# Kernel tuning notes

Hardware: AMD Instinct MI355X
Metric: run time of the kernel (lower is better)

Reference implementation:

```python
import jax, jax.numpy as jnp
import numpy as np

B, C, NQ, NK, S, H, FF = 8, 256, 1024, 4096, 16, 8, 2048
DH = C // H
EPS = 1e-5


def _layernorm(x, g, b):
    m = jnp.mean(x, axis=-1, keepdims=True)
    v = jnp.mean((x - m) ** 2, axis=-1, keepdims=True)
    return (x - m) * jax.lax.rsqrt(v + EPS) * g + b


def _box_query(key_pos, query_pos):
    # key_pos: (B,NK,3); query_pos: (B,NQ,6) = centers ++ box sizes (L,H,W)
    centers = query_pos[:, :, None, :3]            # (B,NQ,1,3)
    half = 0.5 * query_pos[:, :, None, 3:]         # (B,NQ,1,3)
    off = jnp.abs(key_pos[:, None, :, :] - centers)  # (B,NQ,NK,3)
    inside = jnp.all(off <= half, axis=-1)         # (B,NQ,NK)
    # first n_sample inside-points in index order (stable sort: inside first)
    order = jnp.argsort(~inside, axis=-1, stable=True)
    idx = order[..., :S]                           # (B,NQ,S)
    valid = jnp.take_along_axis(inside, idx, axis=-1)
    mask = ~valid                                  # True = padded / masked
    idx = jnp.where(mask, 0, idx)
    mask = mask.at[..., 0].set(False)              # matches cuda path: slot 0 never masked
    return idx, mask


def _forward(query, key, query_pos, key_pos,
             q_w, q_b, k_w, k_b, v_w, v_b, o_w, o_b,
             lin1_w, lin1_b, lin2_w, lin2_b,
             n1_g, n1_b, n2_g, n2_b, qpe_w, qpe_b, kpe_w, kpe_b):
    idx, mask = _box_query(key_pos, query_pos)     # (B,NQ,S), (B,NQ,S)
    # gather neighborhoods
    gxyz = jax.vmap(lambda kp, ix: kp[ix])(key_pos, idx)        # (B,NQ,S,3)
    gxyz = gxyz - query_pos[:, :, None, :3]                     # center-relative
    gfeat = jax.vmap(lambda kf, ix: kf[:, ix])(key, idx)        # (B,C,NQ,S)

    BQ = B * NQ
    kfeat = jnp.transpose(gfeat, (0, 2, 3, 1)).reshape(BQ, S, C)   # (BQ,S,C)
    kpe = gxyz.reshape(BQ, S, 3) @ kpe_w.T + kpe_b                 # cross_embed
    qtok = jnp.transpose(query, (0, 2, 1)).reshape(BQ, C)          # (BQ,C)
    qpe = (query_pos @ qpe_w.T + qpe_b).reshape(BQ, C)             # pos_embed

    # multihead cross-attention: 1 query vs S=16 local keys per group
    kv_in = kfeat + kpe
    qh = ((qtok + qpe) @ q_w.T + q_b).reshape(BQ, H, DH)
    kh = (kv_in @ k_w.T + k_b).reshape(BQ, S, H, DH)
    vh = (kv_in @ v_w.T + v_b).reshape(BQ, S, H, DH)
    scores = jnp.einsum('bhd,bshd->bhs', qh, kh) / np.sqrt(DH)    # (BQ,H,S)
    scores = jnp.where(mask.reshape(BQ, 1, S), -1e30, scores)
    attn = jax.nn.softmax(scores, axis=-1)
    ao = jnp.einsum('bhs,bshd->bhd', attn, vh).reshape(BQ, C)
    ao = ao @ o_w.T + o_b

    x = _layernorm(qtok + ao, n1_g, n1_b)                         # post-norm
    ff = jax.nn.relu(x @ lin1_w.T + lin1_b) @ lin2_w.T + lin2_b
    x = _layernorm(x + ff, n2_g, n2_b)
    return jnp.transpose(x.reshape(B, NQ, C), (0, 2, 1))          # (B,C,NQ)


def setup_inputs() -> dict:
    rng = jax.random.key(0)
    ks = jax.random.split(rng, 24)
    s = 0.02
    query = jax.random.normal(ks[0], (B, C, NQ), jnp.float32)
    key = jax.random.normal(ks[1], (B, C, NK), jnp.float32)
    key_pos = jax.random.uniform(ks[2], (B, NK, 3), jnp.float32)
    centers = jax.random.uniform(ks[3], (B, NQ, 3), jnp.float32)
    sizes = jax.random.uniform(ks[4], (B, NQ, 3), jnp.float32, minval=0.1, maxval=0.4)
    query_pos = jnp.concatenate([centers, sizes], axis=-1)
    p = {
        'q_w': jax.random.normal(ks[5], (C, C)) * s, 'q_b': jnp.zeros((C,)),
        'k_w': jax.random.normal(ks[6], (C, C)) * s, 'k_b': jnp.zeros((C,)),
        'v_w': jax.random.normal(ks[7], (C, C)) * s, 'v_b': jnp.zeros((C,)),
        'o_w': jax.random.normal(ks[8], (C, C)) * s, 'o_b': jnp.zeros((C,)),
        'lin1_w': jax.random.normal(ks[9], (FF, C)) * s, 'lin1_b': jnp.zeros((FF,)),
        'lin2_w': jax.random.normal(ks[10], (C, FF)) * s, 'lin2_b': jnp.zeros((C,)),
        'n1_g': jnp.ones((C,)), 'n1_b': jnp.zeros((C,)),
        'n2_g': jnp.ones((C,)), 'n2_b': jnp.zeros((C,)),
        'qpe_w': jax.random.normal(ks[11], (C, 6)) * s, 'qpe_b': jnp.zeros((C,)),
        'kpe_w': jax.random.normal(ks[12], (C, 3)) * s, 'kpe_b': jnp.zeros((C,)),
    }
    return dict(query=query, key=key, query_pos=query_pos, key_pos=key_pos, **p)


def reference(query, key, query_pos, key_pos,
              q_w, q_b, k_w, k_b, v_w, v_b, o_w, o_b,
              lin1_w, lin1_b, lin2_w, lin2_b,
              n1_g, n1_b, n2_g, n2_b, qpe_w, qpe_b, kpe_w, kpe_b):
    return _forward(query, key, query_pos, key_pos,
                    q_w, q_b, k_w, k_b, v_w, v_b, o_w, o_b,
                    lin1_w, lin1_b, lin2_w, lin2_b,
                    n1_g, n1_b, n2_g, n2_b, qpe_w, qpe_b, kpe_w, kpe_b)
```

## Files before the change

### kernel.cpp

```cpp
#include <hip/hip_runtime.h>
#include <cstdint>

#define B_   8
#define C_   256
#define NQ_  1024
#define NK_  4096
#define S_   16
#define H_   8
#define FF_  2048
#define DH_  32
#define BQ_  (B_*NQ_)
#define EPS_ 1e-5f
#define KS_  8

typedef __bf16 bf16x8 __attribute__((ext_vector_type(8)));
typedef __bf16 bf16x4 __attribute__((ext_vector_type(4)));
typedef float  f32x4  __attribute__((ext_vector_type(4)));

struct CvtArgs {
  const float* src[6];
  __bf16* dst[6];
};

#define SEGA 2048
#define SEGB 10240
#define SEGC 12288
#define SEGD 13568
#define NPREP 13584

__global__ __launch_bounds__(256) void k_prep(
    const float* __restrict__ query, const float* __restrict__ key,
    const float* __restrict__ query_pos, const float* __restrict__ key_pos,
    const float* __restrict__ qpe_w, const float* __restrict__ qpe_b,
    const float* __restrict__ k_w, const float* __restrict__ k_b,
    const float* __restrict__ v_w, const float* __restrict__ v_b,
    const float* __restrict__ kpe_w, const float* __restrict__ kpe_b,
    CvtArgs ca,
    __bf16* __restrict__ keyTb, __bf16* __restrict__ qtokb,
    __bf16* __restrict__ qinb,
    float4* __restrict__ Pk, float4* __restrict__ Pv,
    int* __restrict__ idxo, int* __restrict__ masko) {
  __shared__ __align__(16) float smem[1248];
  int blk = blockIdx.x, t = threadIdx.x;
  int tx = t & 31, ty = t >> 5;

  if (blk < SEGA) {
    int lane = t & 63;
    int q = blk * 4 + (t >> 6);
    int b = q >> 10;
    const float* kpb = key_pos + (size_t)b * NK_ * 3;
    const float* qp = query_pos + (size_t)q * 6;
    float cx = qp[0], cy = qp[1], cz = qp[2];
    float hx = 0.5f * qp[3], hy = 0.5f * qp[4], hz = 0.5f * qp[5];
    int* iq = idxo + (size_t)q * S_;
    int found = 0;
    for (int ch = 0; ch < NK_ / 64; ch += 4) {
      float dx[4], dy[4], dz[4];
#pragma unroll
      for (int u = 0; u < 4; ++u) {
        int k = (ch + u) * 64 + lane;
        dx[u] = fabsf(kpb[k * 3 + 0] - cx);
        dy[u] = fabsf(kpb[k * 3 + 1] - cy);
        dz[u] = fabsf(kpb[k * 3 + 2] - cz);
      }
#pragma unroll
      for (int u = 0; u < 4; ++u) {
        bool inside = (dx[u] <= hx) && (dy[u] <= hy) && (dz[u] <= hz);
        unsigned long long bal = __ballot(inside);
        if (inside) {
          int slot = found + __popcll(bal & ((1ull << lane) - 1ull));
          if (slot < S_) iq[slot] = (ch + u) * 64 + lane;
        }
        found += __popcll(bal);
      }
      if (found >= S_) break;
    }
    if (found > S_) found = S_;
    if (lane < S_) {
      int m = (lane < found) ? 0 : 1;
      if (lane >= found) iq[lane] = 0;
      if (lane == 0) m = 0;
      masko[(size_t)q * S_ + lane] = m;
    }
  } else if (blk < SEGB) {
    int local = blk - SEGA;
    float (*tt)[33] = (float(*)[33])smem;
    int x = local & 127, y = (local >> 7) & 7, z = local >> 10;
    int j0 = x * 32, i0 = y * 32;
    const float* inz = key + (size_t)z * C_ * NK_;
    __bf16* outz = keyTb + (size_t)z * NK_ * C_;
#pragma unroll
    for (int r = 0; r < 32; r += 8)
      tt[ty + r][tx] = inz[(size_t)(i0 + ty + r) * NK_ + (j0 + tx)];
    __syncthreads();
#pragma unroll
    for (int r = 0; r < 32; r += 8)
      outz[(size_t)(j0 + ty + r) * C_ + (i0 + tx)] = (__bf16)tt[tx][ty + r];
  } else if (blk < SEGC) {
    int local = blk - SEGB;
    float (*tt)[33] = (float(*)[33])smem;
    float (*sqp)[6] = (float(*)[6])(smem + 1056);
    int x = local & 31, y = (local >> 5) & 7, z = local >> 8;
    int nq0 = x * 32, c0 = y * 32;
    const float* inz = query + (size_t)z * C_ * NQ_;
#pragma unroll
    for (int r = 0; r < 32; r += 8)
      tt[ty + r][tx] = inz[(size_t)(c0 + ty + r) * NQ_ + (nq0 + tx)];
    if (t < 192)
      sqp[t / 6][t % 6] = query_pos[((size_t)z * NQ_ + nq0 + t / 6) * 6 + (t % 6)];
    int c = c0 + tx;
    float w0 = qpe_w[c * 6 + 0], w1 = qpe_w[c * 6 + 1], w2 = qpe_w[c * 6 + 2];
    float w3 = qpe_w[c * 6 + 3], w4 = qpe_w[c * 6 + 4], w5 = qpe_w[c * 6 + 5];
    float wb = qpe_b[c];
    __syncthreads();
#pragma unroll
    for (int r = 0; r < 32; r += 8) {
      int nql = ty + r;
      size_t row = (size_t)z * NQ_ + nq0 + nql;
      float v = tt[tx][nql];
      float pe = wb + sqp[nql][0] * w0 + sqp[nql][1] * w1 + sqp[nql][2] * w2 +
                 sqp[nql][3] * w3 + sqp[nql][4] * w4 + sqp[nql][5] * w5;
      qtokb[row * C_ + c] = (__bf16)v;
      qinb[row * C_ + c] = (__bf16)(v + pe);
    }
  } else if (blk < SEGD) {
    int local = blk - SEGC;
    int idx, base;
    if (local < 64)       { idx = 0; base = local; }
    else if (local < 128) { idx = 1; base = local - 64; }
    else if (local < 192) { idx = 2; base = local - 128; }
    else if (local < 256) { idx = 3; base = local - 192; }
    else if (local < 768) { idx = 4; base = local - 256; }
    else                  { idx = 5; base = local - 768; }
    size_t off = (size_t)base * 1024 + t * 4;
    float4 v = *(const float4*)(ca.src[idx] + off);
    __bf16* o = ca.dst[idx] + off;
    o[0] = (__bf16)v.x; o[1] = (__bf16)v.y; o[2] = (__bf16)v.z; o[3] = (__bf16)v.w;
  } else {
    int local = blk - SEGD;
    int bx = local & 7, bv = local >> 3;
    const float* w  = bv ? v_w : k_w;
    const float* wb = bv ? v_b : k_b;
    float4* P = bv ? Pv : Pk;
    float4 (*red)[8] = (float4(*)[8])smem;
    int nl = t >> 3, ks = (t & 7) * 32;
    int n = bx * 32 + nl;
    const float* wr = w + (size_t)n * C_;
    float p0 = 0.f, p1 = 0.f, p2 = 0.f, pb = 0.f;
#pragma unroll
    for (int k = ks; k < ks + 32; ++k) {
      float wv = wr[k];
      p0 += kpe_w[k * 3 + 0] * wv;
      p1 += kpe_w[k * 3 + 1] * wv;
      p2 += kpe_w[k * 3 + 2] * wv;
      pb += kpe_b[k] * wv;
    }
    red[nl][t & 7] = make_float4(p0, p1, p2, pb);
    __syncthreads();
    if (t < 32) {
      float4 s = red[t][0];
#pragma unroll
      for (int j = 1; j < 8; ++j) {
        float4 r = red[t][j];
        s.x += r.x; s.y += r.y; s.z += r.z; s.w += r.w;
      }
      s.w += wb[bx * 32 + t];
      P[bx * 32 + t] = s;
    }
  }
}

template <int BM, int BN, int RELU, int OUT_BF16>
__device__ __forceinline__ void gemm_body(
    const __bf16* __restrict__ A, const __bf16* __restrict__ Wn,
    const float* __restrict__ bias, void* __restrict__ outp,
    int n0, int m0, int N, int K, int kbeg, int kend) {
  constexpr int MI = BM / 32, JN = BN / 32;
  constexpr int AIT = (BM * 64) / 2048, BIT = (BN * 64) / 2048;
  __shared__ __bf16 As[BM][72];
  __shared__ __bf16 Bs[BN][72];
  int t = threadIdx.x;
  int lane = t & 63, w = t >> 6;
  int lane16 = lane & 15, quad = lane >> 4;
  int wm = (w & 1) * (BM / 2), wn = (w >> 1) * (BN / 2);

  f32x4 acc[MI][JN];
#pragma unroll
  for (int i = 0; i < MI; ++i)
#pragma unroll
    for (int j = 0; j < JN; ++j) acc[i][j] = (f32x4){0.f, 0.f, 0.f, 0.f};

  for (int k0 = kbeg; k0 < kend; k0 += 64) {
#pragma unroll
    for (int i = 0; i < AIT; ++i) {
      int ii = i * 256 + t;
      int m = ii >> 3, kc = (ii & 7) * 8;
      *(bf16x8*)&As[m][kc] = *(const bf16x8*)&A[(size_t)(m0 + m) * K + k0 + kc];
    }
#pragma unroll
    for (int i = 0; i < BIT; ++i) {
      int ii = i * 256 + t;
      int m = ii >> 3, kc = (ii & 7) * 8;
      *(bf16x8*)&Bs[m][kc] = *(const bf16x8*)&Wn[(size_t)(n0 + m) * K + k0 + kc];
    }
    __syncthreads();
#pragma unroll
    for (int kk = 0; kk < 64; kk += 32) {
      bf16x8 af[MI], bfr[JN];
#pragma unroll
      for (int i = 0; i < MI; ++i)
        af[i] = *(const bf16x8*)&As[wm + i * 16 + lane16][kk + quad * 8];
#pragma unroll
      for (int j = 0; j < JN; ++j)
        bfr[j] = *(const bf16x8*)&Bs[wn + j * 16 + lane16][kk + quad * 8];
#pragma unroll
      for (int i = 0; i < MI; ++i)
#pragma unroll
        for (int j = 0; j < JN; ++j)
          acc[i][j] = __builtin_amdgcn_mfma_f32_16x16x32_bf16(af[i], bfr[j], acc[i][j], 0, 0, 0);
    }
    __syncthreads();
  }

#pragma unroll
  for (int j = 0; j < JN; ++j) {
    int col = n0 + wn + j * 16 + lane16;
    float bv = bias ? bias[col] : 0.f;
#pragma unroll
    for (int i = 0; i < MI; ++i) {
#pragma unroll
      for (int r = 0; r < 4; ++r) {
        int row = m0 + wm + i * 16 + quad * 4 + r;
        float v = acc[i][j][r] + bv;
        if (RELU) v = fmaxf(v, 0.f);
        if (OUT_BF16)
          ((__bf16*)outp)[(size_t)row * N + col] = (__bf16)v;
        else
          ((float*)outp)[(size_t)row * N + col] = v;
      }
    }
  }
}

template <int BM, int BN, int RELU, int OUT_BF16>
__global__ __launch_bounds__(256) void k_gemm(
    const __bf16* __restrict__ A, const __bf16* __restrict__ Wn,
    const float* __restrict__ bias, void* __restrict__ outp, int N, int K) {
  gemm_body<BM, BN, RELU, OUT_BF16>(A, Wn, bias, outp,
                                    blockIdx.x * BN, blockIdx.y * BM, N, K, 0, K);
}

__global__ __launch_bounds__(256) void k_gemmsk(
    const __bf16* __restrict__ A, const __bf16* __restrict__ Wn,
    __bf16* __restrict__ partials) {
  int ks = blockIdx.z;
  int kbeg = ks * (FF_ / KS_), kend = kbeg + FF_ / KS_;
  gemm_body<128, 128, 0, 1>(A, Wn, nullptr,
                            partials + (size_t)ks * BQ_ * C_,
                            blockIdx.x * 128, blockIdx.y * 128, C_, FF_, kbeg, kend);
}

__global__ __launch_bounds__(256) void k_gemmsko(
    const __bf16* __restrict__ A, const __bf16* __restrict__ Wn,
    __bf16* __restrict__ partials) {
  int ks = blockIdx.z;
  int kbeg = ks * 128, kend = kbeg + 128;
  gemm_body<128, 64, 0, 1>(A, Wn, nullptr,
                           partials + (size_t)ks * BQ_ * C_,
                           blockIdx.x * 64, blockIdx.y * 128, C_, C_, kbeg, kend);
}

__global__ __launch_bounds__(256) void k_gemm2(
    const __bf16* __restrict__ keyTb, const __bf16* __restrict__ kvwb,
    __bf16* __restrict__ khvbuf,
    const __bf16* __restrict__ qinb, const __bf16* __restrict__ qwb,
    const float* __restrict__ q_b, __bf16* __restrict__ qhb) {
  int blk = blockIdx.x;
  const __bf16 *A, *Wn; const float* bias; __bf16* outp; int n0, m0, N;
  if (blk < 1024) {
    A = keyTb; Wn = kvwb; bias = nullptr; outp = khvbuf;
    n0 = (blk & 3) * 128; m0 = (blk >> 2) * 128; N = 512;
  } else {
    int l = blk - 1024;
    A = qinb; Wn = qwb; bias = q_b; outp = qhb;
    n0 = (l & 1) * 128; m0 = (l >> 1) * 128; N = 256;
  }
  gemm_body<128, 128, 0, 1>(A, Wn, bias, outp, n0, m0, N, 256, 0, 256);
}

__global__ __launch_bounds__(256) void k_attnf(
    const __bf16* __restrict__ khv,
    const float* __restrict__ key_pos,
    const float* __restrict__ query_pos,
    const int* __restrict__ idx,
    const int* __restrict__ maskb,
    const __bf16* __restrict__ qhb,
    const float4* __restrict__ Pk,
    const float4* __restrict__ Pv,
    __bf16* __restrict__ aob) {
  __shared__ __bf16 kvs[S_][520];
  __shared__ float qrow[C_];
  __shared__ float sc[H_][S_];
  __shared__ float pw[H_][S_];
  __shared__ float4 gx4[S_];
  __shared__ float4 pgxs[H_];
  __shared__ float4 qpks[H_];
  __shared__ int srow[S_], smask[S_];
  int bq = blockIdx.x, b = bq >> 10, t = threadIdx.x;

  if (t < S_) {
    int k = idx[(size_t)bq * S_ + t];
    srow[t] = b * NK_ + k;
    smask[t] = maskb[(size_t)bq * S_ + t];
    const float* kpp = key_pos + ((size_t)b * NK_ + k) * 3;
    const float* qp  = query_pos + (size_t)bq * 6;
    gx4[t] = make_float4(kpp[0] - qp[0], kpp[1] - qp[1], kpp[2] - qp[2], 1.f);
  }
  float qv_t = (float)qhb[(size_t)bq * C_ + t];
  qrow[t] = qv_t;
  {
    float4 p = Pk[t];
    p.x *= qv_t; p.y *= qv_t; p.z *= qv_t; p.w *= qv_t;
#pragma unroll
    for (int off = 16; off >= 1; off >>= 1) {
      p.x += __shfl_xor(p.x, off);
      p.y += __shfl_xor(p.y, off);
      p.z += __shfl_xor(p.z, off);
      p.w += __shfl_xor(p.w, off);
    }
    if ((t & 31) == 0) {
      const float s = 0.17677669529663687f;
      qpks[t >> 5] = make_float4(p.x * s, p.y * s, p.z * s, p.w * s);
    }
  }
  __syncthreads();
  {
    int s = t >> 4, c0 = (t & 15) * 32;
    const __bf16* src = khv + (size_t)srow[s] * 512 + c0;
    *(bf16x8*)&kvs[s][c0]      = *(const bf16x8*)&src[0];
    *(bf16x8*)&kvs[s][c0 + 8]  = *(const bf16x8*)&src[8];
    *(bf16x8*)&kvs[s][c0 + 16] = *(const bf16x8*)&src[16];
    *(bf16x8*)&kvs[s][c0 + 24] = *(const bf16x8*)&src[24];
  }
  __syncthreads();
  if (t < H_ * S_) {
    int h = t >> 4, s = t & (S_ - 1);
    float d = 0.f;
#pragma unroll
    for (int c0 = 0; c0 < 32; c0 += 8) {
      bf16x8 xv = *(const bf16x8*)&kvs[s][h * 32 + c0];
#pragma unroll
      for (int j = 0; j < 8; ++j) d += qrow[h * 32 + c0 + j] * (float)xv[j];
    }
    d *= 0.17677669529663687f;
    float4 g = gx4[s];
    float4 pk = qpks[h];
    d += g.x * pk.x + g.y * pk.y + g.z * pk.z + pk.w;
    if (smask[s]) d = -1e30f;
    sc[h][s] = d;
  }
  __syncthreads();
  if (t < H_) {
    float mx = -3.4e38f;
#pragma unroll
    for (int s = 0; s < S_; ++s) mx = fmaxf(mx, sc[t][s]);
    float e[S_], sum = 0.f;
#pragma unroll
    for (int s = 0; s < S_; ++s) { e[s] = expf(sc[t][s] - mx); sum += e[s]; }
    float inv = 1.f / sum;
    float gxx = 0.f, gyy = 0.f, gzz = 0.f;
#pragma unroll
    for (int s = 0; s < S_; ++s) {
      float p = e[s] * inv;
      pw[t][s] = p;
      float4 g = gx4[s];
      gxx += p * g.x; gyy += p * g.y; gzz += p * g.z;
    }
    pgxs[t] = make_float4(gxx, gyy, gzz, 1.f);
  }
  __syncthreads();
  {
    int h = t >> 5;
    float a = 0.f;
#pragma unroll
    for (int s = 0; s < S_; ++s) a += pw[h][s] * (float)kvs[s][256 + t];
    float4 pv = Pv[t];
    float4 g = pgxs[h];
    a += g.x * pv.x + g.y * pv.y + g.z * pv.z + pv.w;
    aob[(size_t)bq * C_ + t] = (__bf16)a;
  }
}

__global__ __launch_bounds__(256) void k_ln1(const __bf16* __restrict__ xa,
                                             const __bf16* __restrict__ op2,
                                             const float* __restrict__ obias,
                                             const float* __restrict__ g,
                                             const float* __restrict__ bb,
                                             __bf16* __restrict__ outb) {
  int wid = (blockIdx.x * 256 + threadIdx.x) >> 6;
  int lane = threadIdx.x & 63;
  bf16x4 va = *(const bf16x4*)&xa[(size_t)wid * C_ + lane * 4];
  float4 ob4 = *(const float4*)(obias + lane * 4);
  bf16x4 p0 = *(const bf16x4*)&op2[(size_t)wid * C_ + lane * 4];
  bf16x4 p1 = *(const bf16x4*)&op2[(size_t)BQ_ * C_ + (size_t)wid * C_ + lane * 4];
  float x0 = (float)va[0] + ob4.x + (float)p0[0] + (float)p1[0];
  float x1 = (float)va[1] + ob4.y + (float)p0[1] + (float)p1[1];
  float x2 = (float)va[2] + ob4.z + (float)p0[2] + (float)p1[2];
  float x3 = (float)va[3] + ob4.w + (float)p0[3] + (float)p1[3];
  float s = x0 + x1 + x2 + x3;
#pragma unroll
  for (int off = 32; off >= 1; off >>= 1) s += __shfl_xor(s, off);
  float mean = s * (1.f / C_);
  float d0 = x0 - mean, d1 = x1 - mean, d2 = x2 - mean, d3 = x3 - mean;
  float v = d0 * d0 + d1 * d1 + d2 * d2 + d3 * d3;
#pragma unroll
  for (int off = 32; off >= 1; off >>= 1) v += __shfl_xor(v, off);
  float inv = 1.f / sqrtf(v * (1.f / C_) + EPS_);
  float4 g4 = *(const float4*)(g + lane * 4);
  float4 b4 = *(const float4*)(bb + lane * 4);
  __bf16* obp = outb + (size_t)wid * C_ + lane * 4;
  obp[0] = (__bf16)(d0 * inv * g4.x + b4.x);
  obp[1] = (__bf16)(d1 * inv * g4.y + b4.y);
  obp[2] = (__bf16)(d2 * inv * g4.z + b4.z);
  obp[3] = (__bf16)(d3 * inv * g4.w + b4.w);
}

__global__ __launch_bounds__(256) void k_lnt(const __bf16* __restrict__ x1b,
                                             const __bf16* __restrict__ ff2p,
                                             const float* __restrict__ l2bias,
                                             const float* __restrict__ g,
                                             const float* __restrict__ bb,
                                             float* __restrict__ out) {
  __shared__ float buf[32][257];
  int z = blockIdx.y, nq0 = blockIdx.x * 32;
  int t = threadIdx.x;
  int w = t >> 6, lane = t & 63;
  float4 g4 = *(const float4*)(g + lane * 4);
  float4 b4 = *(const float4*)(bb + lane * 4);
  float4 l2b = *(const float4*)(l2bias + lane * 4);
#pragma unroll
  for (int rr = 0; rr < 8; ++rr) {
    int row = w * 8 + rr;
    size_t grow = (size_t)z * NQ_ + nq0 + row;
    bf16x4 va = *(const bf16x4*)&x1b[grow * C_ + lane * 4];
    float x0 = (float)va[0] + l2b.x, x1 = (float)va[1] + l2b.y;
    float x2 = (float)va[2] + l2b.z, x3 = (float)va[3] + l2b.w;
#pragma unroll
    for (int ks = 0; ks < KS_; ++ks) {
      bf16x4 p = *(const bf16x4*)&ff2p[((size_t)ks * BQ_ + grow) * C_ + lane * 4];
      x0 += (float)p[0]; x1 += (float)p[1]; x2 += (float)p[2]; x3 += (float)p[3];
    }
    float s = x0 + x1 + x2 + x3;
#pragma unroll
    for (int off = 32; off >= 1; off >>= 1) s += __shfl_xor(s, off);
    float mean = s * (1.f / C_);
    float d0 = x0 - mean, d1 = x1 - mean, d2 = x2 - mean, d3 = x3 - mean;
    float v = d0 * d0 + d1 * d1 + d2 * d2 + d3 * d3;
#pragma unroll
    for (int off = 32; off >= 1; off >>= 1) v += __shfl_xor(v, off);
    float inv = 1.f / sqrtf(v * (1.f / C_) + EPS_);
    buf[row][lane * 4 + 0] = d0 * inv * g4.x + b4.x;
    buf[row][lane * 4 + 1] = d1 * inv * g4.y + b4.y;
    buf[row][lane * 4 + 2] = d2 * inv * g4.z + b4.z;
    buf[row][lane * 4 + 3] = d3 * inv * g4.w + b4.w;
  }
  __syncthreads();
  int tx = t & 31, ty = t >> 5;
#pragma unroll
  for (int ci = 0; ci < 32; ++ci) {
    int c = ci * 8 + ty;
    out[((size_t)z * C_ + c) * NQ_ + nq0 + tx] = buf[tx][c];
  }
}

extern "C" void kernel_launch(void* const* d_in, const int* in_sizes, int n_in,
                              void* d_out, int out_size, void* d_ws, size_t ws_size,
                              hipStream_t stream) {
  const float* query     = (const float*)d_in[0];
  const float* key       = (const float*)d_in[1];
  const float* query_pos = (const float*)d_in[2];
  const float* key_pos   = (const float*)d_in[3];
  const float* q_w = (const float*)d_in[4];  const float* q_b = (const float*)d_in[5];
  const float* k_w = (const float*)d_in[6];  const float* k_b = (const float*)d_in[7];
  const float* v_w = (const float*)d_in[8];  const float* v_b = (const float*)d_in[9];
  const float* o_w = (const float*)d_in[10]; const float* o_b = (const float*)d_in[11];
  const float* lin1_w = (const float*)d_in[12]; const float* lin1_b = (const float*)d_in[13];
  const float* lin2_w = (const float*)d_in[14]; const float* lin2_b = (const float*)d_in[15];
  const float* n1_g = (const float*)d_in[16]; const float* n1_b = (const float*)d_in[17];
  const float* n2_g = (const float*)d_in[18]; const float* n2_b = (const float*)d_in[19];
  const float* qpe_w = (const float*)d_in[20]; const float* qpe_b = (const float*)d_in[21];
  const float* kpe_w = (const float*)d_in[22]; const float* kpe_b = (const float*)d_in[23];
  float* out = (float*)d_out;

  const size_t BQc = (size_t)BQ_ * C_;
  float* w = (float*)d_ws;
  size_t o = 0;
  __bf16* keyTb = (__bf16*)(w + o); o += (size_t)B_ * NK_ * C_ / 2;
  __bf16* qtokb = (__bf16*)(w + o); o += BQc / 2;
  __bf16* op2  = (__bf16*)(w + o); o += BQc;
  __bf16* khvbuf = (__bf16*)(w + o); o += (size_t)B_ * NK_ * 512 / 2;
  __bf16* ff2p = (__bf16*)(w + o); o += BQc * KS_ / 2;
  __bf16* qinb = (__bf16*)(w + o); o += BQc / 2;
  __bf16* qhb  = (__bf16*)(w + o); o += BQc / 2;
  __bf16* aob  = (__bf16*)(w + o); o += BQc / 2;
  __bf16* x1b  = (__bf16*)(w + o); o += BQc / 2;
  __bf16* qwb  = (__bf16*)(w + o); o += (size_t)C_ * C_ / 2;
  __bf16* kvwb = (__bf16*)(w + o); o += (size_t)C_ * C_;
  __bf16* owb  = (__bf16*)(w + o); o += (size_t)C_ * C_ / 2;
  __bf16* l1b  = (__bf16*)(w + o); o += (size_t)C_ * FF_ / 2;
  __bf16* l2b  = (__bf16*)(w + o); o += (size_t)C_ * FF_ / 2;
  float4* Pk   = (float4*)(w + o); o += C_ * 4;
  float4* Pv   = (float4*)(w + o); o += C_ * 4;
  int* idxb  = (int*)(w + o); o += (size_t)BQ_ * S_;
  int* maskb = (int*)(w + o); o += (size_t)BQ_ * S_;
  __bf16* ff1b = khvbuf;

  CvtArgs ca;
  ca.src[0] = q_w; ca.dst[0] = qwb;
  ca.src[1] = k_w; ca.dst[1] = kvwb;
  ca.src[2] = v_w; ca.dst[2] = kvwb + (size_t)C_ * C_;
  ca.src[3] = o_w; ca.dst[3] = owb;
  ca.src[4] = lin1_w; ca.dst[4] = l1b;
  ca.src[5] = lin2_w; ca.dst[5] = l2b;
  k_prep<<<NPREP, 256, 0, stream>>>(query, key, query_pos, key_pos,
                                    qpe_w, qpe_b, k_w, k_b, v_w, v_b,
                                    kpe_w, kpe_b, ca,
                                    keyTb, qtokb, qinb, Pk, Pv, idxb, maskb);
  k_gemm2<<<1024 + 128, 256, 0, stream>>>(keyTb, kvwb, khvbuf, qinb, qwb, q_b, qhb);
  k_attnf<<<BQ_, 256, 0, stream>>>(khvbuf, key_pos, query_pos, idxb, maskb,
                                   qhb, Pk, Pv, aob);
  k_gemmsko<<<dim3(C_ / 64, BQ_ / 128, 2), 256, 0, stream>>>(aob, owb, op2);
  k_ln1<<<BQ_ / 4, 256, 0, stream>>>(qtokb, op2, o_b, n1_g, n1_b, x1b);
  k_gemm<128, 128, 1, 1><<<dim3(FF_ / 128, BQ_ / 128), 256, 0, stream>>>(
      x1b, l1b, lin1_b, ff1b, FF_, C_);
  k_gemmsk<<<dim3(C_ / 128, BQ_ / 128, KS_), 256, 0, stream>>>(ff1b, l2b, ff2p);
  k_lnt<<<dim3(NQ_ / 32, B_), 256, 0, stream>>>(x1b, ff2p, lin2_b, n2_g, n2_b, out);
}
```

Measured before the change: 258.6 us.

## Fuse key transpose and bf16 conversion into K/V projection GEMM A-loads

Removes the separate transpose-and-convert stage that wrote a bf16 transposed copy of the key tensor, and the buffer that held it. The K/V projection GEMM now reads fp32 key directly in its channel-major layout, converting to bf16 in registers as it builds the MFMA A fragments, while only the weight tile goes through shared memory. This avoids a full write and re-read of the key tensor. In exchange the A operand is loaded without shared-memory staging or vectorization, as eight scalar strided fp32 loads per fragment. Those loads are coalesced across lanes but may be less efficient than the tuned GEMM body.

After: 266.1 us. 1.03x slower.

```diff
diff --git a/kernel.cpp b/kernel.cpp
--- a/kernel.cpp
+++ b/kernel.cpp
@@ -23,21 +23,19 @@
 };
 
 #define SEGA 2048
-#define SEGB 10240
-#define SEGC 12288
-#define SEGD 13568
-#define NPREP 13584
+#define SEGB 4096
+#define SEGC 5376
+#define NPREP 5392
 
 __global__ __launch_bounds__(256) void k_prep(
-    const float* __restrict__ query, const float* __restrict__ key,
+    const float* __restrict__ query,
     const float* __restrict__ query_pos, const float* __restrict__ key_pos,
     const float* __restrict__ qpe_w, const float* __restrict__ qpe_b,
     const float* __restrict__ k_w, const float* __restrict__ k_b,
     const float* __restrict__ v_w, const float* __restrict__ v_b,
     const float* __restrict__ kpe_w, const float* __restrict__ kpe_b,
     CvtArgs ca,
-    __bf16* __restrict__ keyTb, __bf16* __restrict__ qtokb,
-    __bf16* __restrict__ qinb,
+    __bf16* __restrict__ qtokb, __bf16* __restrict__ qinb,
     float4* __restrict__ Pk, float4* __restrict__ Pv,
     int* __restrict__ idxo, int* __restrict__ masko) {
   __shared__ __align__(16) float smem[1248];
@@ -85,20 +83,6 @@
   } else if (blk < SEGB) {
     int local = blk - SEGA;
     float (*tt)[33] = (float(*)[33])smem;
-    int x = local & 127, y = (local >> 7) & 7, z = local >> 10;
-    int j0 = x * 32, i0 = y * 32;
-    const float* inz = key + (size_t)z * C_ * NK_;
-    __bf16* outz = keyTb + (size_t)z * NK_ * C_;
-#pragma unroll
-    for (int r = 0; r < 32; r += 8)
-      tt[ty + r][tx] = inz[(size_t)(i0 + ty + r) * NK_ + (j0 + tx)];
-    __syncthreads();
-#pragma unroll
-    for (int r = 0; r < 32; r += 8)
-      outz[(size_t)(j0 + ty + r) * C_ + (i0 + tx)] = (__bf16)tt[tx][ty + r];
-  } else if (blk < SEGC) {
-    int local = blk - SEGB;
-    float (*tt)[33] = (float(*)[33])smem;
     float (*sqp)[6] = (float(*)[6])(smem + 1056);
     int x = local & 31, y = (local >> 5) & 7, z = local >> 8;
     int nq0 = x * 32, c0 = y * 32;
@@ -123,8 +107,8 @@
       qtokb[row * C_ + c] = (__bf16)v;
       qinb[row * C_ + c] = (__bf16)(v + pe);
     }
-  } else if (blk < SEGD) {
-    int local = blk - SEGC;
+  } else if (blk < SEGC) {
+    int local = blk - SEGB;
     int idx, base;
     if (local < 64)       { idx = 0; base = local; }
     else if (local < 128) { idx = 1; base = local - 64; }
@@ -137,7 +121,7 @@
     __bf16* o = ca.dst[idx] + off;
     o[0] = (__bf16)v.x; o[1] = (__bf16)v.y; o[2] = (__bf16)v.z; o[3] = (__bf16)v.w;
   } else {
-    int local = blk - SEGD;
+    int local = blk - SEGC;
     int bx = local & 7, bv = local >> 3;
     const float* w  = bv ? v_w : k_w;
     const float* wb = bv ? v_b : k_b;
@@ -271,21 +255,75 @@
 }
 
 __global__ __launch_bounds__(256) void k_gemm2(
-    const __bf16* __restrict__ keyTb, const __bf16* __restrict__ kvwb,
+    const float* __restrict__ key, const __bf16* __restrict__ kvwb,
     __bf16* __restrict__ khvbuf,
     const __bf16* __restrict__ qinb, const __bf16* __restrict__ qwb,
     const float* __restrict__ q_b, __bf16* __restrict__ qhb) {
   int blk = blockIdx.x;
-  const __bf16 *A, *Wn; const float* bias; __bf16* outp; int n0, m0, N;
   if (blk < 1024) {
-    A = keyTb; Wn = kvwb; bias = nullptr; outp = khvbuf;
-    n0 = (blk & 3) * 128; m0 = (blk >> 2) * 128; N = 512;
+    __shared__ __bf16 Bs[128][72];
+    int n0 = (blk & 3) * 128, m0 = (blk >> 2) * 128;
+    int t = threadIdx.x;
+    int lane = t & 63, w = t >> 6;
+    int lane16 = lane & 15, quad = lane >> 4;
+    int wm = (w & 1) * 64, wn = (w >> 1) * 64;
+    int b = m0 >> 12;
+    int nk0 = m0 & (NK_ - 1);
+    const float* keyz = key + (size_t)b * C_ * NK_;
+
+    f32x4 acc[4][4];
+#pragma unroll
+    for (int i = 0; i < 4; ++i)
+#pragma unroll
+      for (int j = 0; j < 4; ++j) acc[i][j] = (f32x4){0.f, 0.f, 0.f, 0.f};
+
+    for (int k0 = 0; k0 < C_; k0 += 64) {
+#pragma unroll
+      for (int i = 0; i < 4; ++i) {
+        int ii = i * 256 + t;
+        int m = ii >> 3, kc = (ii & 7) * 8;
+        *(bf16x8*)&Bs[m][kc] = *(const bf16x8*)&kvwb[(size_t)(n0 + m) * C_ + k0 + kc];
+      }
+      __syncthreads();
+#pragma unroll
+      for (int kk = 0; kk < 64; kk += 32) {
+        bf16x8 af[4], bfr[4];
+#pragma unroll
+        for (int i = 0; i < 4; ++i) {
+          const float* ap = keyz + (size_t)(k0 + kk + quad * 8) * NK_ +
+                            (nk0 + wm + i * 16 + lane16);
+#pragma unroll
+          for (int j = 0; j < 8; ++j)
+            af[i][j] = (__bf16)ap[(size_t)j * NK_];
+        }
+#pragma unroll
+        for (int j = 0; j < 4; ++j)
+          bfr[j] = *(const bf16x8*)&Bs[wn + j * 16 + lane16][kk + quad * 8];
+#pragma unroll
+        for (int i = 0; i < 4; ++i)
+#pragma unroll
+          for (int j = 0; j < 4; ++j)
+            acc[i][j] = __builtin_amdgcn_mfma_f32_16x16x32_bf16(af[i], bfr[j], acc[i][j], 0, 0, 0);
+      }
+      __syncthreads();
+    }
+#pragma unroll
+    for (int j = 0; j < 4; ++j) {
+      int col = n0 + wn + j * 16 + lane16;
+#pragma unroll
+      for (int i = 0; i < 4; ++i) {
+#pragma unroll
+        for (int r = 0; r < 4; ++r) {
+          int row = m0 + wm + i * 16 + quad * 4 + r;
+          khvbuf[(size_t)row * 512 + col] = (__bf16)acc[i][j][r];
+        }
+      }
+    }
   } else {
     int l = blk - 1024;
-    A = qinb; Wn = qwb; bias = q_b; outp = qhb;
-    n0 = (l & 1) * 128; m0 = (l >> 1) * 128; N = 256;
-  }
-  gemm_body<128, 128, 0, 1>(A, Wn, bias, outp, n0, m0, N, 256, 0, 256);
+    gemm_body<128, 128, 0, 1>(qinb, qwb, q_b, qhb,
+                              (l & 1) * 128, (l >> 1) * 128, C_, C_, 0, C_);
+  }
 }
 
 __global__ __launch_bounds__(256) void k_attnf(
@@ -495,7 +533,6 @@
   const size_t BQc = (size_t)BQ_ * C_;
   float* w = (float*)d_ws;
   size_t o = 0;
-  __bf16* keyTb = (__bf16*)(w + o); o += (size_t)B_ * NK_ * C_ / 2;
   __bf16* qtokb = (__bf16*)(w + o); o += BQc / 2;
   __bf16* op2  = (__bf16*)(w + o); o += BQc;
   __bf16* khvbuf = (__bf16*)(w + o); o += (size_t)B_ * NK_ * 512 / 2;
@@ -522,11 +559,11 @@
   ca.src[3] = o_w; ca.dst[3] = owb;
   ca.src[4] = lin1_w; ca.dst[4] = l1b;
   ca.src[5] = lin2_w; ca.dst[5] = l2b;
-  k_prep<<<NPREP, 256, 0, stream>>>(query, key, query_pos, key_pos,
+  k_prep<<<NPREP, 256, 0, stream>>>(query, query_pos, key_pos,
                                     qpe_w, qpe_b, k_w, k_b, v_w, v_b,
                                     kpe_w, kpe_b, ca,
-                                    keyTb, qtokb, qinb, Pk, Pv, idxb, maskb);
-  k_gemm2<<<1024 + 128, 256, 0, stream>>>(keyTb, kvwb, khvbuf, qinb, qwb, q_b, qhb);
+                                    qtokb, qinb, Pk, Pv, idxb, maskb);
+  k_gemm2<<<1024 + 128, 256, 0, stream>>>(key, kvwb, khvbuf, qinb, qwb, q_b, qhb);
   k_attnf<<<BQ_, 256, 0, stream>>>(khvbuf, key_pos, query_pos, idxb, maskb,
                                    qhb, Pk, Pv, aob);
   k_gemmsko<<<dim3(C_ / 64, BQ_ / 128, 2), 256, 0, stream>>>(aob, owb, op2);
```
